# Optimization experiments

Measured on AMD Instinct MI355X. Metric: run time of the kernel, lower is better.

The kernel has to match this reference:

```python
import jax, jax.numpy as jnp
import numpy as np

PAD = 1
STRIDE = 1
DIL = 1


def _conv(x, w, b):
    # plain stride-1, pad-1 conv, NCHW / OIHW
    y = jax.lax.conv_general_dilated(x, w, (STRIDE, STRIDE), [(PAD, PAD), (PAD, PAD)],
                                     rhs_dilation=(DIL, DIL),
                                     dimension_numbers=('NCHW', 'OIHW', 'NCHW'))
    return y + b[None, :, None, None]


def _deform_conv2d(x, offset, mask, w_reg):
    # x: [B,C,H,W]; offset: [B,2K,Ho,Wo] (y,x interleaved per kernel tap, torchvision layout)
    # mask: [B,K,Ho,Wo]; w_reg: [O,C,kh,kw]
    B, C, H, W = x.shape
    O, _, kh, kw = w_reg.shape
    K = kh * kw
    Ho, Wo = offset.shape[2], offset.shape[3]

    off = offset.reshape(B, K, 2, Ho, Wo)
    off_y, off_x = off[:, :, 0], off[:, :, 1]  # [B,K,Ho,Wo]

    ki = jnp.arange(K) // kw
    kj = jnp.arange(K) % kw
    base_y = (jnp.arange(Ho) * STRIDE - PAD)[None, :] + (ki * DIL)[:, None]  # [K,Ho]
    base_x = (jnp.arange(Wo) * STRIDE - PAD)[None, :] + (kj * DIL)[:, None]  # [K,Wo]

    py = base_y[None, :, :, None] + off_y  # [B,K,Ho,Wo] fractional sample coords
    px = base_x[None, :, None, :] + off_x

    y0 = jnp.floor(py)
    x0 = jnp.floor(px)
    wy1 = py - y0  # bilinear weights
    wx1 = px - x0
    wy0 = 1.0 - wy1
    wx0 = 1.0 - wx1

    x_flat = x.reshape(B, C, H * W)

    def gather(iy, ix):
        # zero padding outside the image
        valid = (iy >= 0) & (iy < H) & (ix >= 0) & (ix < W)
        iyc = jnp.clip(iy, 0, H - 1).astype(jnp.int32)
        ixc = jnp.clip(ix, 0, W - 1).astype(jnp.int32)
        idx = (iyc * W + ixc).reshape(B, 1, K * Ho * Wo)
        v = jnp.take_along_axis(x_flat, idx, axis=2).reshape(B, C, K, Ho, Wo)
        return v * valid.astype(x.dtype)[:, None]

    y0i = y0.astype(jnp.int32)
    x0i = x0.astype(jnp.int32)
    val = (gather(y0i, x0i) * (wy0 * wx0)[:, None]
           + gather(y0i, x0i + 1) * (wy0 * wx1)[:, None]
           + gather(y0i + 1, x0i) * (wy1 * wx0)[:, None]
           + gather(y0i + 1, x0i + 1) * (wy1 * wx1)[:, None])  # [B,C,K,Ho,Wo]

    val = val * mask[:, None]  # modulated
    # implicit GEMM over (c,k)
    return jnp.einsum('ock,bckhw->bohw', w_reg.reshape(O, C, K), val)


def setup_inputs() -> dict:
    key = jax.random.key(0)
    ks = jax.random.split(key, 7)
    B, C, O, H, W, k = 4, 128, 128, 128, 128, 3
    K = k * k
    x = jax.random.normal(ks[0], (B, C, H, W), dtype=jnp.float32)
    # small random offset/modulator weights (original inits to zero, which would
    # degenerate to a plain conv; small values keep offsets O(1) pixels)
    w_off = jax.random.normal(ks[1], (2 * K, C, k, k), dtype=jnp.float32) * 0.01
    b_off = jax.random.normal(ks[2], (2 * K,), dtype=jnp.float32) * 0.1
    w_mod = jax.random.normal(ks[3], (K, C, k, k), dtype=jnp.float32) * 0.01
    b_mod = jax.random.normal(ks[4], (K,), dtype=jnp.float32) * 0.1
    fan_in = C * K
    w_reg = jax.random.normal(ks[5], (O, C, k, k), dtype=jnp.float32) * (1.0 / np.sqrt(fan_in))
    return {"x": x, "w_off": w_off, "b_off": b_off, "w_mod": w_mod, "b_mod": b_mod, "w_reg": w_reg}


def reference(x, w_off, b_off, w_mod, b_mod, w_reg):
    offset = _conv(x, w_off, b_off)                      # [B,2K,Ho,Wo]
    mask = 2.0 * jax.nn.sigmoid(_conv(x, w_mod, b_mod))  # [B,K,Ho,Wo]
    return _deform_conv2d(x, offset, mask, w_reg)
```

## Files before the change

kernel.cpp:

```cpp
#include <hip/hip_runtime.h>
#include <math.h>

#define HWD 16384
#define NB  4
#define NC  128
#define NO  128

typedef float  f32x4  __attribute__((ext_vector_type(4)));
typedef short  s16x8  __attribute__((ext_vector_type(8)));

__global__ void k_split_wreg(const float* __restrict__ w_reg,
                             short* __restrict__ wA_hi, short* __restrict__ wA_lo) {
    int i = blockIdx.x * 256 + threadIdx.x;
    if (i >= 147456) return;
    int kk = i & 31, o = (i >> 5) & 127, s = i >> 12;
    int cc = s & 3, kt = s >> 2;
    int c  = cc * 32 + kk;
    float w = w_reg[o * 1152 + c * 9 + kt];
    unsigned ub = __builtin_bit_cast(unsigned, w);
    unsigned short h = (unsigned short)(ub >> 16);
    float wh = __builtin_bit_cast(float, (unsigned)h << 16);
    float r  = w - wh;
    unsigned short l = (unsigned short)(__builtin_bit_cast(unsigned, r) >> 16);
    wA_hi[i] = (short)h;
    wA_lo[i] = (short)l;
}

__global__ void k_transpose_wom(const float* __restrict__ w_off, const float* __restrict__ w_mod,
                                float* __restrict__ wt_om) {
    int i = blockIdx.x * 256 + threadIdx.x;
    if (i >= 1152 * 27) return;
    int oc = i % 27, r = i / 27;
    wt_om[i] = (oc < 18) ? w_off[oc * 1152 + r] : w_mod[(oc - 18) * 1152 + r];
}

__global__ __launch_bounds__(256) void k_conv_om(const float* __restrict__ x,
                                                 const float* __restrict__ wt_om,
                                                 float* __restrict__ cbuf) {
    __shared__ float xt[4 * 324];
    int z = blockIdx.z;
    int b     = z / 6;
    int og    = z % 3;
    int chalf = (z % 6) / 3;
    int ty = blockIdx.y * 16, tx = blockIdx.x * 16;
    int tid = threadIdx.x;
    int row = tid >> 4, col = tid & 15;

    float acc[9];
#pragma unroll
    for (int j = 0; j < 9; ++j) acc[j] = 0.f;

    int cbeg = chalf * 64;
    for (int c0 = cbeg; c0 < cbeg + 64; c0 += 4) {
        __syncthreads();
        for (int i = tid; i < 1296; i += 256) {
            int ch = i / 324, rem = i - ch * 324;
            int ry = rem / 18, rx = rem - ry * 18;
            int gy = ty - 1 + ry, gx = tx - 1 + rx;
            float v = 0.f;
            if (gy >= 0 && gy < 128 && gx >= 0 && gx < 128)
                v = x[(((b << 7) + c0 + ch) << 14) + (gy << 7) + gx];
            xt[i] = v;
        }
        __syncthreads();
#pragma unroll
        for (int cc = 0; cc < 4; ++cc) {
#pragma unroll
            for (int k = 0; k < 9; ++k) {
                float xv = xt[cc * 324 + (row + k / 3) * 18 + (col + k % 3)];
                const float* wp = wt_om + ((c0 + cc) * 9 + k) * 27 + og * 9;
#pragma unroll
                for (int j = 0; j < 9; ++j) acc[j] = fmaf(wp[j], xv, acc[j]);
            }
        }
    }

    int hw = ((ty + row) << 7) + tx + col;
#pragma unroll
    for (int j = 0; j < 9; ++j) {
        int oc = og * 9 + j;
        atomicAdd(&cbuf[((b * 27 + oc) << 14) + hw], acc[j]);
    }
}

__global__ __launch_bounds__(256, 4) void k_deform(const float* __restrict__ x,
                                                   const float* __restrict__ cbuf,
                                                   const float* __restrict__ b_off,
                                                   const float* __restrict__ b_mod,
                                                   const short* __restrict__ wA_hi,
                                                   const short* __restrict__ wA_lo,
                                                   float* __restrict__ out) {
    __shared__ int   sp_off[9 * 4 * 64];
    __shared__ float sp_w  [9 * 4 * 64];
    __shared__ short vt_hi[2][64 * 40];
    __shared__ short vt_lo[2][64 * 40];

    int tid = threadIdx.x;
    int b = blockIdx.y;
    int hwbase = blockIdx.x * 64;
    int lane = tid & 63;
    int wid = tid >> 6;

    for (int i = tid; i < 576; i += 256) {
        int k = i >> 6, p = i & 63;
        int hw = hwbase + p;
        int h = hw >> 7, cc = hw & 127;
        const float* cb = cbuf + ((size_t)(b * 27) << 14);
        float oy = cb[((2 * k) << 14) + hw]     + b_off[2 * k];
        float ox = cb[((2 * k + 1) << 14) + hw] + b_off[2 * k + 1];
        float mr = cb[((18 + k) << 14) + hw]    + b_mod[k];
        float m  = 2.f / (1.f + expf(-mr));
        float py = (float)(h - 1 + k / 3) + oy;
        float px = (float)(cc - 1 + k % 3) + ox;
        float fy = floorf(py), fx = floorf(px);
        float wy1 = py - fy, wx1 = px - fx;
        int y0 = (int)fy, x0 = (int)fx;
#pragma unroll
        for (int dy = 0; dy < 2; ++dy)
#pragma unroll
            for (int dx = 0; dx < 2; ++dx) {
                int yy = y0 + dy, xx = x0 + dx;
                bool valid = (yy >= 0) && (yy < 128) && (xx >= 0) && (xx < 128);
                float wgt = m * (dy ? wy1 : 1.f - wy1) * (dx ? wx1 : 1.f - wx1);
                int yc = min(max(yy, 0), 127), xc = min(max(xx, 0), 127);
                int s = (k * 4 + dy * 2 + dx) * 64 + p;
                sp_off[s] = ((yc << 7) + xc) << 2;
                sp_w[s]   = valid ? wgt : 0.f;
            }
    }
    __syncthreads();

    f32x4 acc0[4], acc1[4];
#pragma unroll
    for (int i = 0; i < 4; ++i) { acc0[i] = (f32x4)(0.f); acc1[i] = (f32x4)(0.f); }

    const char* xbase = (const char*)x + ((size_t)b << 23);
    int gpx  = tid & 63;
    int kk0  = (tid >> 6) << 3;
    int albase = (wid * 32 + (lane & 15)) * 32 + ((lane >> 4) << 3);
    int blds   = (lane & 15) * 40 + ((lane >> 4) << 3);

    int buf = 0;
    for (int kt = 0; kt < 9; ++kt) {
        int so = kt * 256 + gpx;
        int   o0 = sp_off[so], o1 = sp_off[so + 64], o2 = sp_off[so + 128], o3 = sp_off[so + 192];
        float s0 = sp_w[so],   s1 = sp_w[so + 64],   s2 = sp_w[so + 128],  s3 = sp_w[so + 192];

        for (int cc = 0; cc < 4; ++cc) {
            int s = kt * 4 + cc;

            s16x8 hi8, lo8;
#pragma unroll
            for (int i = 0; i < 8; ++i) {
                const char* xp = xbase + ((size_t)(cc * 32 + kk0 + i) << 16);
                float v = s0 * *(const float*)(xp + o0);
                v = fmaf(s1, *(const float*)(xp + o1), v);
                v = fmaf(s2, *(const float*)(xp + o2), v);
                v = fmaf(s3, *(const float*)(xp + o3), v);
                unsigned ub = __builtin_bit_cast(unsigned, v);
                unsigned short h = (unsigned short)(ub >> 16);
                float vh = __builtin_bit_cast(float, (unsigned)h << 16);
                float rr = v - vh;
                unsigned short l = (unsigned short)(__builtin_bit_cast(unsigned, rr) >> 16);
                hi8[i] = (short)h;
                lo8[i] = (short)l;
            }
            *(s16x8*)&vt_hi[buf][gpx * 40 + kk0] = hi8;
            *(s16x8*)&vt_lo[buf][gpx * 40 + kk0] = lo8;

            __syncthreads();

            const s16x8* pah = (const s16x8*)(wA_hi + s * 4096 + albase);
            const s16x8* pal = (const s16x8*)(wA_lo + s * 4096 + albase);
            s16x8 a_h0 = pah[0], a_h1 = pah[64];
            s16x8 a_l0 = pal[0], a_l1 = pal[64];
#pragma unroll
            for (int pt = 0; pt < 4; ++pt) {
                s16x8 b_h = *(const s16x8*)&vt_hi[buf][pt * 640 + blds];
                s16x8 b_l = *(const s16x8*)&vt_lo[buf][pt * 640 + blds];
                acc0[pt] = __builtin_amdgcn_mfma_f32_16x16x32_bf16(a_h0, b_h, acc0[pt], 0, 0, 0);
                acc0[pt] = __builtin_amdgcn_mfma_f32_16x16x32_bf16(a_h0, b_l, acc0[pt], 0, 0, 0);
                acc0[pt] = __builtin_amdgcn_mfma_f32_16x16x32_bf16(a_l0, b_h, acc0[pt], 0, 0, 0);
                acc1[pt] = __builtin_amdgcn_mfma_f32_16x16x32_bf16(a_h1, b_h, acc1[pt], 0, 0, 0);
                acc1[pt] = __builtin_amdgcn_mfma_f32_16x16x32_bf16(a_h1, b_l, acc1[pt], 0, 0, 0);
                acc1[pt] = __builtin_amdgcn_mfma_f32_16x16x32_bf16(a_l1, b_h, acc1[pt], 0, 0, 0);
            }
            buf ^= 1;
        }
    }

    int q = lane >> 4, pcol = lane & 15;
#pragma unroll
    for (int pt = 0; pt < 4; ++pt) {
#pragma unroll
        for (int j = 0; j < 4; ++j) {
            int o0_ = wid * 32 + q * 4 + j;
            int o1_ = o0_ + 16;
            int px  = pt * 16 + pcol;
            out[((size_t)(b * NO + o0_) << 14) + hwbase + px] = acc0[pt][j];
            out[((size_t)(b * NO + o1_) << 14) + hwbase + px] = acc1[pt][j];
        }
    }
}

extern "C" void kernel_launch(void* const* d_in, const int* in_sizes, int n_in,
                              void* d_out, int out_size, void* d_ws, size_t ws_size,
                              hipStream_t stream) {
    const float* x     = (const float*)d_in[0];
    const float* w_off = (const float*)d_in[1];
    const float* b_off = (const float*)d_in[2];
    const float* w_mod = (const float*)d_in[3];
    const float* b_mod = (const float*)d_in[4];
    const float* w_reg = (const float*)d_in[5];
    float* out = (float*)d_out;

    float* cbuf  = (float*)d_ws;
    float* wt_om = cbuf + (size_t)NB * 27 * HWD;
    short* wA_hi = (short*)(wt_om + 31104);
    short* wA_lo = wA_hi + 147456;

    hipMemsetAsync(cbuf, 0, (size_t)NB * 27 * HWD * sizeof(float), stream);
    hipLaunchKernelGGL(k_split_wreg,    dim3(576), dim3(256), 0, stream, w_reg, wA_hi, wA_lo);
    hipLaunchKernelGGL(k_transpose_wom, dim3(122), dim3(256), 0, stream, w_off, w_mod, wt_om);
    hipLaunchKernelGGL(k_conv_om, dim3(8, 8, NB * 6), dim3(256), 0, stream, x, wt_om, cbuf);
    hipLaunchKernelGGL(k_deform, dim3(HWD / 64, NB), dim3(256), 0, stream,
                       x, cbuf, b_off, b_mod, wA_hi, wA_lo, out);
}
```

Baseline: 430.5 us.

## Restructure offset conv and deform gather with loop reorder, LDS swizzle, XCD mapping

The offset/mask conv now has each thread compute all 27 output channels for one pixel, splits the channels into two halves and reduces them in shared memory. This drops the memset and the global atomics. The deform kernel swaps its loop order so channel chunks are outer and kernel taps inner, and the weight split layout is changed to match. It also issues all 32 gather loads before the arithmetic, adds an XOR swizzle to the shared-memory B tile to avoid bank conflicts, and remaps block IDs so each XCD handles one batch half to improve L2 locality. The costs are higher register pressure (27 accumulators and 32 raw values) and a conv grid of only 256 blocks.

```diff
diff --git a/kernel.cpp b/kernel.cpp
--- a/kernel.cpp
+++ b/kernel.cpp
@@ -14,7 +14,7 @@
     int i = blockIdx.x * 256 + threadIdx.x;
     if (i >= 147456) return;
     int kk = i & 31, o = (i >> 5) & 127, s = i >> 12;
-    int cc = s & 3, kt = s >> 2;
+    int cc = s / 9, kt = s % 9;
     int c  = cc * 32 + kk;
     float w = w_reg[o * 1152 + c * 9 + kt];
     unsigned ub = __builtin_bit_cast(unsigned, w);
@@ -34,52 +34,55 @@
     wt_om[i] = (oc < 18) ? w_off[oc * 1152 + r] : w_mod[(oc - 18) * 1152 + r];
 }
 
-__global__ __launch_bounds__(256) void k_conv_om(const float* __restrict__ x,
+__global__ __launch_bounds__(512) void k_conv_om(const float* __restrict__ x,
                                                  const float* __restrict__ wt_om,
                                                  float* __restrict__ cbuf) {
-    __shared__ float xt[4 * 324];
-    int z = blockIdx.z;
-    int b     = z / 6;
-    int og    = z % 3;
-    int chalf = (z % 6) / 3;
-    int ty = blockIdx.y * 16, tx = blockIdx.x * 16;
+    __shared__ float sred[27 * 256];
     int tid = threadIdx.x;
-    int row = tid >> 4, col = tid & 15;
-
-    float acc[9];
-#pragma unroll
-    for (int j = 0; j < 9; ++j) acc[j] = 0.f;
-
-    int cbeg = chalf * 64;
-    for (int c0 = cbeg; c0 < cbeg + 64; c0 += 4) {
-        __syncthreads();
-        for (int i = tid; i < 1296; i += 256) {
-            int ch = i / 324, rem = i - ch * 324;
-            int ry = rem / 18, rx = rem - ry * 18;
-            int gy = ty - 1 + ry, gx = tx - 1 + rx;
-            float v = 0.f;
-            if (gy >= 0 && gy < 128 && gx >= 0 && gx < 128)
-                v = x[(((b << 7) + c0 + ch) << 14) + (gy << 7) + gx];
-            xt[i] = v;
-        }
-        __syncthreads();
-#pragma unroll
-        for (int cc = 0; cc < 4; ++cc) {
-#pragma unroll
-            for (int k = 0; k < 9; ++k) {
-                float xv = xt[cc * 324 + (row + k / 3) * 18 + (col + k % 3)];
-                const float* wp = wt_om + ((c0 + cc) * 9 + k) * 27 + og * 9;
-#pragma unroll
-                for (int j = 0; j < 9; ++j) acc[j] = fmaf(wp[j], xv, acc[j]);
-            }
-        }
-    }
-
-    int hw = ((ty + row) << 7) + tx + col;
-#pragma unroll
-    for (int j = 0; j < 9; ++j) {
-        int oc = og * 9 + j;
-        atomicAdd(&cbuf[((b * 27 + oc) << 14) + hw], acc[j]);
+    int t = tid & 255;
+    int chalf = tid >> 8;
+    int pxg = blockIdx.x;
+    int b   = pxg >> 6;
+    int hw  = ((pxg & 63) << 8) + t;
+    int h = hw >> 7, wcol = hw & 127;
+
+    int offs[9]; float msk[9];
+#pragma unroll
+    for (int k = 0; k < 9; ++k) {
+        int gy = h + k / 3 - 1, gx = wcol + k % 3 - 1;
+        bool vv = (gy >= 0) && (gy < 128) && (gx >= 0) && (gx < 128);
+        int cy = min(max(gy, 0), 127), cx = min(max(gx, 0), 127);
+        offs[k] = (cy << 7) + cx;
+        msk[k]  = vv ? 1.f : 0.f;
+    }
+
+    float acc[27];
+#pragma unroll
+    for (int j = 0; j < 27; ++j) acc[j] = 0.f;
+
+    const float* xb = x + ((size_t)(b * NC + chalf * 64) << 14);
+    for (int c = 0; c < 64; ++c) {
+        const float* xp = xb + ((size_t)c << 14);
+        float v[9];
+#pragma unroll
+        for (int k = 0; k < 9; ++k) v[k] = xp[offs[k]] * msk[k];
+        const float* wp = wt_om + (size_t)(chalf * 64 + c) * 9 * 27;
+#pragma unroll
+        for (int k = 0; k < 9; ++k)
+#pragma unroll
+            for (int j = 0; j < 27; ++j)
+                acc[j] = fmaf(wp[k * 27 + j], v[k], acc[j]);
+    }
+
+    if (chalf == 1) {
+#pragma unroll
+        for (int j = 0; j < 27; ++j) sred[j * 256 + t] = acc[j];
+    }
+    __syncthreads();
+    if (chalf == 0) {
+#pragma unroll
+        for (int j = 0; j < 27; ++j)
+            cbuf[((size_t)(b * 27 + j) << 14) + hw] = acc[j] + sred[j * 256 + t];
     }
 }
 
@@ -96,8 +99,12 @@
     __shared__ short vt_lo[2][64 * 40];
 
     int tid = threadIdx.x;
-    int b = blockIdx.y;
-    int hwbase = blockIdx.x * 64;
+    int bid = blockIdx.x;
+    int xcd  = bid & 7;
+    int b    = xcd >> 1;
+    int half = xcd & 1;
+    int strip = half * 128 + (bid >> 3);
+    int hwbase = strip * 64;
     int lane = tid & 63;
     int wid = tid >> 6;
 
@@ -138,25 +145,35 @@
     int gpx  = tid & 63;
     int kk0  = (tid >> 6) << 3;
     int albase = (wid * 32 + (lane & 15)) * 32 + ((lane >> 4) << 3);
-    int blds   = (lane & 15) * 40 + ((lane >> 4) << 3);
+    int welem = gpx * 40 + (((kk0 >> 3) ^ ((gpx >> 3) & 3)) << 3);
 
     int buf = 0;
-    for (int kt = 0; kt < 9; ++kt) {
-        int so = kt * 256 + gpx;
-        int   o0 = sp_off[so], o1 = sp_off[so + 64], o2 = sp_off[so + 128], o3 = sp_off[so + 192];
-        float s0 = sp_w[so],   s1 = sp_w[so + 64],   s2 = sp_w[so + 128],  s3 = sp_w[so + 192];
-
-        for (int cc = 0; cc < 4; ++cc) {
-            int s = kt * 4 + cc;
-
+    for (int cc = 0; cc < 4; ++cc) {
+        const char* xc0 = xbase + ((size_t)(cc * 32 + kk0) << 16);
+#pragma unroll
+        for (int kt = 0; kt < 9; ++kt) {
+            int s = cc * 9 + kt;
+
+            int so = kt * 256 + gpx;
+            int   o0 = sp_off[so], o1 = sp_off[so + 64], o2 = sp_off[so + 128], o3 = sp_off[so + 192];
+            float s0 = sp_w[so],   s1 = sp_w[so + 64],   s2 = sp_w[so + 128],  s3 = sp_w[so + 192];
+
+            float raw[32];
+#pragma unroll
+            for (int i = 0; i < 8; ++i) {
+                const char* xp = xc0 + ((size_t)i << 16);
+                raw[i * 4 + 0] = *(const float*)(xp + o0);
+                raw[i * 4 + 1] = *(const float*)(xp + o1);
+                raw[i * 4 + 2] = *(const float*)(xp + o2);
+                raw[i * 4 + 3] = *(const float*)(xp + o3);
+            }
             s16x8 hi8, lo8;
 #pragma unroll
             for (int i = 0; i < 8; ++i) {
-                const char* xp = xbase + ((size_t)(cc * 32 + kk0 + i) << 16);
-                float v = s0 * *(const float*)(xp + o0);
-                v = fmaf(s1, *(const float*)(xp + o1), v);
-                v = fmaf(s2, *(const float*)(xp + o2), v);
-                v = fmaf(s3, *(const float*)(xp + o3), v);
+                float v = s0 * raw[i * 4 + 0];
+                v = fmaf(s1, raw[i * 4 + 1], v);
+                v = fmaf(s2, raw[i * 4 + 2], v);
+                v = fmaf(s3, raw[i * 4 + 3], v);
                 unsigned ub = __builtin_bit_cast(unsigned, v);
                 unsigned short h = (unsigned short)(ub >> 16);
                 float vh = __builtin_bit_cast(float, (unsigned)h << 16);
@@ -165,8 +182,8 @@
                 hi8[i] = (short)h;
                 lo8[i] = (short)l;
             }
-            *(s16x8*)&vt_hi[buf][gpx * 40 + kk0] = hi8;
-            *(s16x8*)&vt_lo[buf][gpx * 40 + kk0] = lo8;
+            *(s16x8*)&vt_hi[buf][welem] = hi8;
+            *(s16x8*)&vt_lo[buf][welem] = lo8;
 
             __syncthreads();
 
@@ -176,8 +193,10 @@
             s16x8 a_l0 = pal[0], a_l1 = pal[64];
 #pragma unroll
             for (int pt = 0; pt < 4; ++pt) {
-                s16x8 b_h = *(const s16x8*)&vt_hi[buf][pt * 640 + blds];
-                s16x8 b_l = *(const s16x8*)&vt_lo[buf][pt * 640 + blds];
+                int prow = pt * 16 + (lane & 15);
+                int relem = prow * 40 + ((((lane >> 4)) ^ ((prow >> 3) & 3)) << 3);
+                s16x8 b_h = *(const s16x8*)&vt_hi[buf][relem];
+                s16x8 b_l = *(const s16x8*)&vt_lo[buf][relem];
                 acc0[pt] = __builtin_amdgcn_mfma_f32_16x16x32_bf16(a_h0, b_h, acc0[pt], 0, 0, 0);
                 acc0[pt] = __builtin_amdgcn_mfma_f32_16x16x32_bf16(a_h0, b_l, acc0[pt], 0, 0, 0);
                 acc0[pt] = __builtin_amdgcn_mfma_f32_16x16x32_bf16(a_l0, b_h, acc0[pt], 0, 0, 0);
@@ -219,10 +238,9 @@
     short* wA_hi = (short*)(wt_om + 31104);
     short* wA_lo = wA_hi + 147456;
 
-    hipMemsetAsync(cbuf, 0, (size_t)NB * 27 * HWD * sizeof(float), stream);
     hipLaunchKernelGGL(k_split_wreg,    dim3(576), dim3(256), 0, stream, w_reg, wA_hi, wA_lo);
     hipLaunchKernelGGL(k_transpose_wom, dim3(122), dim3(256), 0, stream, w_off, w_mod, wt_om);
-    hipLaunchKernelGGL(k_conv_om, dim3(8, 8, NB * 6), dim3(256), 0, stream, x, wt_om, cbuf);
-    hipLaunchKernelGGL(k_deform, dim3(HWD / 64, NB), dim3(256), 0, stream,
+    hipLaunchKernelGGL(k_conv_om, dim3(256), dim3(512), 0, stream, x, wt_om, cbuf);
+    hipLaunchKernelGGL(k_deform, dim3(1024), dim3(256), 0, stream,
                        x, cbuf, b_off, b_mod, wA_hi, wA_lo, out);
 }
```

New measurement: 590.7 us. 1.37x slower.
